# Kernel optimization log

Hardware: AMD Instinct MI355X
Metric: run time of the kernel (lower is better)

Reference implementation:

```python
import jax, jax.numpy as jnp
import numpy as np

BLOCK = 16
NVFP4_LEVELS = jnp.array([0.0, 0.5, 1.0, 1.5, 2.0, 3.0, 4.0, 6.0], dtype=jnp.float32)


def _quantize_to_nvfp4(x_blocks):
    # x_blocks: [n_blocks, BLOCK]
    amax = jnp.clip(jnp.max(jnp.abs(x_blocks), axis=-1, keepdims=True), 1e-12, None)
    scale = amax / 6.0
    x_norm = jnp.abs(x_blocks) / scale
    idx = jnp.argmin(jnp.abs(x_norm[..., None] - NVFP4_LEVELS), axis=-1)
    return jnp.sign(x_blocks) * NVFP4_LEVELS[idx] * scale


def setup_inputs() -> dict:
    key = jax.random.key(0)
    k1, k2, k3, k4 = jax.random.split(key, 4)
    B, S, H, O = 16, 1024, 1152, 4608
    x = jax.random.normal(k1, (B, S, H), dtype=jnp.float32)
    w_quantized = jax.random.normal(k2, (O, H), dtype=jnp.float32) * 0.02
    smooth_scale = jax.random.uniform(k3, (H,), dtype=jnp.float32, minval=0.5, maxval=2.0)
    bias = jax.random.normal(k4, (O,), dtype=jnp.float32) * 0.02
    return {"x": x, "w_quantized": w_quantized, "smooth_scale": smooth_scale, "bias": bias}


def reference(x, w_quantized, smooth_scale, bias):
    orig_shape = x.shape
    H = orig_shape[-1]
    # SmoothQuant activation prescale
    x_s = (x * smooth_scale).reshape(-1, H)              # [T, H]
    # per-token prescale to [-6, 6]
    token_max = jnp.clip(jnp.max(jnp.abs(x_s), axis=-1, keepdims=True), 1e-12, None)
    pre_scale = token_max / 6.0
    x_pre = x_s / pre_scale
    # blockwise NVFP4 fake quant
    x_q = _quantize_to_nvfp4(x_pre.reshape(-1, BLOCK)).reshape(x_s.shape)
    x_q = x_q * pre_scale                                # restore token scale
    out = x_q.reshape(orig_shape) @ w_quantized.T + bias  # F.linear
    return out
```

## Files before the change

kernel.cpp:

```cpp
#include <hip/hip_runtime.h>
#include <hip/hip_bf16.h>

typedef __attribute__((ext_vector_type(8))) __bf16 bf16x8;
typedef __attribute__((ext_vector_type(4))) float  f32x4;

#define H_DIM 1152

__global__ __launch_bounds__(128) void quant_kernel(
    const float* __restrict__ x, const float* __restrict__ smooth,
    unsigned short* __restrict__ xq)
{
    __shared__ float xs[H_DIM];
    __shared__ float wmax_s[2];
    const int t = blockIdx.x;
    const int tid = threadIdx.x;
    const float* xrow = x + (size_t)t * H_DIM;

    float m = 0.f;
    for (int i = tid; i < H_DIM; i += 128) {
        float v = xrow[i] * smooth[i];
        xs[i] = v;
        m = fmaxf(m, fabsf(v));
    }
    for (int off = 32; off > 0; off >>= 1)
        m = fmaxf(m, __shfl_xor(m, off, 64));
    if ((tid & 63) == 0) wmax_s[tid >> 6] = m;
    __syncthreads();

    const float token_max = fmaxf(fmaxf(wmax_s[0], wmax_s[1]), 1e-12f);
    const float pre_scale = token_max / 6.0f;

    if (tid < H_DIM / 16) {
        const int base = tid * 16;
        float vals[16];
        float amax = 0.f;
        for (int j = 0; j < 16; ++j) {
            float v = xs[base + j] / pre_scale;
            vals[j] = v;
            amax = fmaxf(amax, fabsf(v));
        }
        amax = fmaxf(amax, 1e-12f);
        const float scale = amax / 6.0f;
        alignas(16) __hip_bfloat16 outv[16];
        for (int j = 0; j < 16; ++j) {
            float av = fabsf(vals[j]);
            float xn = av / scale;
            float lvl = xn <= 0.25f ? 0.0f
                      : xn <= 0.75f ? 0.5f
                      : xn <= 1.25f ? 1.0f
                      : xn <= 1.75f ? 1.5f
                      : xn <= 2.5f  ? 2.0f
                      : xn <= 3.5f  ? 3.0f
                      : xn <= 5.0f  ? 4.0f : 6.0f;
            float q = copysignf(lvl * scale, vals[j]) * pre_scale;
            outv[j] = __float2bfloat16(q);
        }
        uint4* dst = (uint4*)(xq + (size_t)t * H_DIM + base);
        dst[0] = *(const uint4*)&outv[0];
        dst[1] = *(const uint4*)&outv[8];
    }
}

__global__ __launch_bounds__(256) void wconv_kernel(
    const float* __restrict__ w, unsigned short* __restrict__ wq, int n)
{
    int i = (blockIdx.x * 256 + threadIdx.x) * 4;
    if (i < n) {
        float4 v = *(const float4*)(w + i);
        alignas(8) __hip_bfloat16 o[4];
        o[0] = __float2bfloat16(v.x);
        o[1] = __float2bfloat16(v.y);
        o[2] = __float2bfloat16(v.z);
        o[3] = __float2bfloat16(v.w);
        *(uint2*)(wq + i) = *(const uint2*)o;
    }
}

__device__ __forceinline__ void async_copy16(const void* gptr, void* lptr)
{
    __builtin_amdgcn_global_load_lds(
        (const __attribute__((address_space(1))) unsigned int*)gptr,
        (__attribute__((address_space(3))) unsigned int*)lptr,
        16, 0, 0);
}

__global__ __launch_bounds__(256) void gemm_bt_kernel(
    const unsigned short* __restrict__ A,
    const unsigned short* __restrict__ B,
    const float* __restrict__ bias,
    float* __restrict__ C,
    int M, int N, int K)
{
    __shared__ unsigned short sA[128 * 32];
    __shared__ unsigned short sB[128 * 32];

    const int tid  = threadIdx.x;
    const int wave = tid >> 6;
    const int lane = tid & 63;
    const int m0 = blockIdx.y * 128;
    const int n0 = blockIdx.x * 128;
    const int wave_m = (wave & 1) * 64;
    const int wave_n = (wave >> 1) * 64;
    const int lane16 = lane & 15;
    const int quad   = lane >> 4;

    const int rowA = lane >> 2;
    const int colA = (lane & 3) * 8;

    f32x4 acc[4][4] = {};

    for (int k0 = 0; k0 < K; k0 += 32) {
        __syncthreads();
        #pragma unroll
        for (int s = 0; s < 2; ++s) {
            const int R = wave * 32 + s * 16;
            async_copy16(A + (size_t)(m0 + R + rowA) * K + k0 + colA, sA + R * 32);
            async_copy16(B + (size_t)(n0 + R + rowA) * K + k0 + colA, sB + R * 32);
        }
        __syncthreads();

        bf16x8 a[4], b[4];
        #pragma unroll
        for (int i = 0; i < 4; ++i)
            a[i] = *(const bf16x8*)(sA + (wave_m + i * 16 + lane16) * 32 + quad * 8);
        #pragma unroll
        for (int j = 0; j < 4; ++j)
            b[j] = *(const bf16x8*)(sB + (wave_n + j * 16 + lane16) * 32 + quad * 8);
        #pragma unroll
        for (int i = 0; i < 4; ++i)
            #pragma unroll
            for (int j = 0; j < 4; ++j)
                acc[i][j] = __builtin_amdgcn_mfma_f32_16x16x32_bf16(a[i], b[j], acc[i][j], 0, 0, 0);
    }

    #pragma unroll
    for (int i = 0; i < 4; ++i) {
        const int m = m0 + wave_m + i * 16 + quad * 4;
        #pragma unroll
        for (int j = 0; j < 4; ++j) {
            const int n = n0 + wave_n + j * 16 + lane16;
            const float bv = bias[n];
            float* cp = C + (size_t)m * N + n;
            #pragma unroll
            for (int r = 0; r < 4; ++r)
                cp[(size_t)r * N] = acc[i][j][r] + bv;
        }
    }
}

extern "C" void kernel_launch(void* const* d_in, const int* in_sizes, int n_in,
                              void* d_out, int out_size, void* d_ws, size_t ws_size,
                              hipStream_t stream)
{
    const float* x      = (const float*)d_in[0];
    const float* w      = (const float*)d_in[1];
    const float* smooth = (const float*)d_in[2];
    const float* bias   = (const float*)d_in[3];
    float* out = (float*)d_out;

    const int H = in_sizes[2];
    const int T = in_sizes[0] / H;
    const int O = in_sizes[3];

    unsigned short* xq = (unsigned short*)d_ws;
    unsigned short* wq = (unsigned short*)((char*)d_ws + (size_t)T * H * sizeof(unsigned short));

    quant_kernel<<<T, 128, 0, stream>>>(x, smooth, xq);
    wconv_kernel<<<(O * H / 4 + 255) / 256, 256, 0, stream>>>(w, wq, O * H);

    dim3 grid(O / 128, T / 128);
    gemm_bt_kernel<<<grid, 256, 0, stream>>>(xq, wq, bias, out, T, O, H);
}
```

Baseline: 577.4 us.

## Switch GEMM operands to fp16 and rewrite quant kernel as single-wave vectorized

Changes the intermediate activation and weight format from bf16 to fp16 and uses the fp16 MFMA instruction, which gives more mantissa precision at the same throughput. The quantization kernel becomes one 64-lane wave per token, loading float4 from registers with no shared memory and no block barrier, and reducing each 16-element block max with lane shuffles. This cuts the quant kernel's overhead. fp16 could overflow for very large activation values.

```diff
diff --git a/kernel.cpp b/kernel.cpp
--- a/kernel.cpp
+++ b/kernel.cpp
@@ -1,77 +1,94 @@
 #include <hip/hip_runtime.h>
 #include <hip/hip_bf16.h>
 
-typedef __attribute__((ext_vector_type(8))) __bf16 bf16x8;
+typedef __attribute__((ext_vector_type(8))) _Float16 f16x8;
 typedef __attribute__((ext_vector_type(4))) float  f32x4;
 
 #define H_DIM 1152
+#define H_VEC (H_DIM / 4)
 
-__global__ __launch_bounds__(128) void quant_kernel(
-    const float* __restrict__ x, const float* __restrict__ smooth,
-    unsigned short* __restrict__ xq)
+__device__ __forceinline__ float nvfp4_level(float xn) {
+    return xn <= 0.25f ? 0.0f
+         : xn <= 0.75f ? 0.5f
+         : xn <= 1.25f ? 1.0f
+         : xn <= 1.75f ? 1.5f
+         : xn <= 2.5f  ? 2.0f
+         : xn <= 3.5f  ? 3.0f
+         : xn <= 5.0f  ? 4.0f : 6.0f;
+}
+
+__global__ __launch_bounds__(64) void quant_kernel(
+    const float4* __restrict__ x4, const float4* __restrict__ s4,
+    _Float16* __restrict__ xq)
 {
-    __shared__ float xs[H_DIM];
-    __shared__ float wmax_s[2];
-    const int t = blockIdx.x;
-    const int tid = threadIdx.x;
-    const float* xrow = x + (size_t)t * H_DIM;
+    const int t    = blockIdx.x;
+    const int lane = threadIdx.x;
+    const float4* xrow = x4 + (size_t)t * H_VEC;
 
-    float m = 0.f;
-    for (int i = tid; i < H_DIM; i += 128) {
-        float v = xrow[i] * smooth[i];
-        xs[i] = v;
-        m = fmaxf(m, fabsf(v));
+    float4 v[5];
+    int    fidx[5];
+    float  m = 0.f;
+    #pragma unroll
+    for (int i = 0; i < 5; ++i) {
+        const int f = (i < 4) ? (lane + 64 * i) : (256 + (lane & 31));
+        fidx[i] = f;
+        const float4 xx = xrow[f];
+        const float4 ss = s4[f];
+        float4 vv;
+        vv.x = xx.x * ss.x; vv.y = xx.y * ss.y;
+        vv.z = xx.z * ss.z; vv.w = xx.w * ss.w;
+        v[i] = vv;
+        m = fmaxf(m, fmaxf(fmaxf(fabsf(vv.x), fabsf(vv.y)),
+                           fmaxf(fabsf(vv.z), fabsf(vv.w))));
     }
-    for (int off = 32; off > 0; off >>= 1)
+    #pragma unroll
+    for (int off = 32; off; off >>= 1)
         m = fmaxf(m, __shfl_xor(m, off, 64));
-    if ((tid & 63) == 0) wmax_s[tid >> 6] = m;
-    __syncthreads();
+    const float pre_scale = fmaxf(m, 1e-12f) / 6.0f;
 
-    const float token_max = fmaxf(fmaxf(wmax_s[0], wmax_s[1]), 1e-12f);
-    const float pre_scale = token_max / 6.0f;
+    #pragma unroll
+    for (int i = 0; i < 5; ++i) {
+        float4 p;
+        p.x = v[i].x / pre_scale;
+        p.y = v[i].y / pre_scale;
+        p.z = v[i].z / pre_scale;
+        p.w = v[i].w / pre_scale;
+        float g = fmaxf(fmaxf(fabsf(p.x), fabsf(p.y)),
+                        fmaxf(fabsf(p.z), fabsf(p.w)));
+        g = fmaxf(g, __shfl_xor(g, 1, 64));
+        g = fmaxf(g, __shfl_xor(g, 2, 64));
+        const float scale = fmaxf(g, 1e-12f) / 6.0f;
 
-    if (tid < H_DIM / 16) {
-        const int base = tid * 16;
-        float vals[16];
-        float amax = 0.f;
-        for (int j = 0; j < 16; ++j) {
-            float v = xs[base + j] / pre_scale;
-            vals[j] = v;
-            amax = fmaxf(amax, fabsf(v));
+        alignas(8) _Float16 o[4];
+        {
+            float q;
+            q = copysignf(nvfp4_level(fabsf(p.x) / scale) * scale, p.x) * pre_scale;
+            o[0] = (_Float16)q;
+            q = copysignf(nvfp4_level(fabsf(p.y) / scale) * scale, p.y) * pre_scale;
+            o[1] = (_Float16)q;
+            q = copysignf(nvfp4_level(fabsf(p.z) / scale) * scale, p.z) * pre_scale;
+            o[2] = (_Float16)q;
+            q = copysignf(nvfp4_level(fabsf(p.w) / scale) * scale, p.w) * pre_scale;
+            o[3] = (_Float16)q;
         }
-        amax = fmaxf(amax, 1e-12f);
-        const float scale = amax / 6.0f;
-        alignas(16) __hip_bfloat16 outv[16];
-        for (int j = 0; j < 16; ++j) {
-            float av = fabsf(vals[j]);
-            float xn = av / scale;
-            float lvl = xn <= 0.25f ? 0.0f
-                      : xn <= 0.75f ? 0.5f
-                      : xn <= 1.25f ? 1.0f
-                      : xn <= 1.75f ? 1.5f
-                      : xn <= 2.5f  ? 2.0f
-                      : xn <= 3.5f  ? 3.0f
-                      : xn <= 5.0f  ? 4.0f : 6.0f;
-            float q = copysignf(lvl * scale, vals[j]) * pre_scale;
-            outv[j] = __float2bfloat16(q);
+        if (i < 4 || lane < 32) {
+            _Float16* dst = xq + (size_t)t * H_DIM + fidx[i] * 4;
+            *(uint2*)dst = *(const uint2*)o;
         }
-        uint4* dst = (uint4*)(xq + (size_t)t * H_DIM + base);
-        dst[0] = *(const uint4*)&outv[0];
-        dst[1] = *(const uint4*)&outv[8];
     }
 }
 
 __global__ __launch_bounds__(256) void wconv_kernel(
-    const float* __restrict__ w, unsigned short* __restrict__ wq, int n)
+    const float* __restrict__ w, _Float16* __restrict__ wq, int n)
 {
     int i = (blockIdx.x * 256 + threadIdx.x) * 4;
     if (i < n) {
         float4 v = *(const float4*)(w + i);
-        alignas(8) __hip_bfloat16 o[4];
-        o[0] = __float2bfloat16(v.x);
-        o[1] = __float2bfloat16(v.y);
-        o[2] = __float2bfloat16(v.z);
-        o[3] = __float2bfloat16(v.w);
+        alignas(8) _Float16 o[4];
+        o[0] = (_Float16)v.x;
+        o[1] = (_Float16)v.y;
+        o[2] = (_Float16)v.z;
+        o[3] = (_Float16)v.w;
         *(uint2*)(wq + i) = *(const uint2*)o;
     }
 }
@@ -85,14 +102,14 @@
 }
 
 __global__ __launch_bounds__(256) void gemm_bt_kernel(
-    const unsigned short* __restrict__ A,
-    const unsigned short* __restrict__ B,
+    const _Float16* __restrict__ A,
+    const _Float16* __restrict__ B,
     const float* __restrict__ bias,
     float* __restrict__ C,
     int M, int N, int K)
 {
-    __shared__ unsigned short sA[128 * 32];
-    __shared__ unsigned short sB[128 * 32];
+    __shared__ _Float16 sA[128 * 32];
+    __shared__ _Float16 sB[128 * 32];
 
     const int tid  = threadIdx.x;
     const int wave = tid >> 6;
@@ -119,18 +136,18 @@
         }
         __syncthreads();
 
-        bf16x8 a[4], b[4];
+        f16x8 a[4], b[4];
         #pragma unroll
         for (int i = 0; i < 4; ++i)
-            a[i] = *(const bf16x8*)(sA + (wave_m + i * 16 + lane16) * 32 + quad * 8);
+            a[i] = *(const f16x8*)(sA + (wave_m + i * 16 + lane16) * 32 + quad * 8);
         #pragma unroll
         for (int j = 0; j < 4; ++j)
-            b[j] = *(const bf16x8*)(sB + (wave_n + j * 16 + lane16) * 32 + quad * 8);
+            b[j] = *(const f16x8*)(sB + (wave_n + j * 16 + lane16) * 32 + quad * 8);
         #pragma unroll
         for (int i = 0; i < 4; ++i)
             #pragma unroll
             for (int j = 0; j < 4; ++j)
-                acc[i][j] = __builtin_amdgcn_mfma_f32_16x16x32_bf16(a[i], b[j], acc[i][j], 0, 0, 0);
+                acc[i][j] = __builtin_amdgcn_mfma_f32_16x16x32_f16(a[i], b[j], acc[i][j], 0, 0, 0);
     }
 
     #pragma unroll
@@ -162,10 +179,10 @@
     const int T = in_sizes[0] / H;
     const int O = in_sizes[3];
 
-    unsigned short* xq = (unsigned short*)d_ws;
-    unsigned short* wq = (unsigned short*)((char*)d_ws + (size_t)T * H * sizeof(unsigned short));
+    _Float16* xq = (_Float16*)d_ws;
+    _Float16* wq = (_Float16*)((char*)d_ws + (size_t)T * H * sizeof(_Float16));
 
-    quant_kernel<<<T, 128, 0, stream>>>(x, smooth, xq);
+    quant_kernel<<<T, 64, 0, stream>>>((const float4*)x, (const float4*)smooth, xq);
     wconv_kernel<<<(O * H / 4 + 255) / 256, 256, 0, stream>>>(w, wq, O * H);
 
     dim3 grid(O / 128, T / 128);
```

After: 569.6 us. About the same (-1.4%).
